# Performance work log

Hardware: AMD Instinct MI355X
Metric: run time of the kernel (lower is better)

## Reference

```python
import jax, jax.numpy as jnp
import numpy as np

N = 100000          # num_nodes
E = 1250000         # num_edges
H = 64              # node_hidden_size
T = 2               # num_rounds


def setup_inputs() -> dict:
    key = jax.random.key(0)
    ks = jax.random.split(key, 10)
    s = 0.1  # init scale for weights
    return {
        "x": jax.random.normal(ks[0], (N, H), dtype=jnp.float32),
        "edge_index": jax.random.randint(ks[1], (2, E), 0, N, dtype=jnp.int64),
        "edge_attr": jax.random.normal(ks[2], (E, 1), dtype=jnp.float32),
        # message layers: Linear(2H+1 -> H), one per round
        "msg_W": jax.random.normal(ks[3], (T, H, 2 * H + 1), dtype=jnp.float32) * s,
        "msg_b": jax.random.normal(ks[4], (T, H), dtype=jnp.float32) * s,
        # GRUCell params, gate order (r, z, n) as in torch
        "gru_Wih": jax.random.normal(ks[5], (T, 3 * H, H), dtype=jnp.float32) * s,
        "gru_bih": jax.random.normal(ks[6], (T, 3 * H), dtype=jnp.float32) * s,
        "gru_Whh": jax.random.normal(ks[7], (T, 3 * H, H), dtype=jnp.float32) * s,
        "gru_bhh": jax.random.normal(ks[8], (T, 3 * H), dtype=jnp.float32) * s,
    }


def _gru_cell(inp, h, Wih, bih, Whh, bhh):
    # torch.nn.GRUCell math, gate order r, z, n
    gi = inp @ Wih.T + bih   # [N, 3H]
    gh = h @ Whh.T + bhh     # [N, 3H]
    i_r, i_z, i_n = jnp.split(gi, 3, axis=1)
    h_r, h_z, h_n = jnp.split(gh, 3, axis=1)
    r = jax.nn.sigmoid(i_r + h_r)
    z = jax.nn.sigmoid(i_z + h_z)
    n = jnp.tanh(i_n + r * h_n)
    return (1.0 - z) * n + z * h


def reference(x, edge_index, edge_attr, msg_W, msg_b, gru_Wih, gru_bih, gru_Whh, gru_bhh):
    row, col = edge_index[0], edge_index[1]
    num_rounds = msg_W.shape[0]
    for t in range(num_rounds):
        src = x[row]    # [E, H]
        dest = x[col]   # [E, H]
        m_input = jnp.concatenate([dest, src, edge_attr], axis=1)  # [E, 2H+1]
        messages = m_input @ msg_W[t].T + msg_b[t]                 # [E, H]
        agg = jax.ops.segment_sum(messages, row, num_segments=x.shape[0])  # [N, H]
        x = _gru_cell(agg, x, gru_Wih[t], gru_bih[t], gru_Whh[t], gru_bhh[t])
    return x
```

## Files before the change

### kernel.cpp

```cpp
#include <hip/hip_runtime.h>
#include <hip/hip_bf16.h>
#include <hip/hip_fp16.h>

#define H 64
#define CAP 48

typedef __attribute__((ext_vector_type(8))) short short8;
typedef __attribute__((ext_vector_type(4))) float float4v;

__device__ __forceinline__ short f2bf_bits(float f) {
    union { __hip_bfloat16 b; short s; } u;
    u.b = __float2bfloat16(f);
    return u.s;
}
__device__ __forceinline__ float bf2f(unsigned short s) {
    union { unsigned int u; float f; } v;
    v.u = ((unsigned int)s) << 16;
    return v.f;
}
__device__ __forceinline__ void split8(const float* p, short8& hi, short8& lo) {
    float4v f0 = *(const float4v*)p;
    float4v f1 = *(const float4v*)(p + 4);
#pragma unroll
    for (int j = 0; j < 8; j++) {
        float f = (j < 4) ? f0[j] : f1[j - 4];
        short h = f2bf_bits(f);
        float fh = bf2f((unsigned short)h);
        hi[j] = h;
        lo[j] = f2bf_bits(f - fh);
    }
}
__device__ __forceinline__ void zero8(short8& hi, short8& lo) {
#pragma unroll
    for (int j = 0; j < 8; j++) { hi[j] = 0; lo[j] = 0; }
}

#define MFMA(a, b, c) __builtin_amdgcn_mfma_f32_16x16x32_bf16(a, b, c, 0, 0, 0)

__global__ __launch_bounds__(256) void count_prep(
    const int* __restrict__ row, int* __restrict__ deg, int* __restrict__ lpos,
    int E, int EB,
    const float* __restrict__ msg_W,
    const float* __restrict__ Wih, const float* __restrict__ Whh,
    short* __restrict__ msgfrag, short* __restrict__ grufrag, int T)
{
    if ((int)blockIdx.x < EB) {
        int e = blockIdx.x * 256 + threadIdx.x;
        if (e < E) lpos[e] = atomicAdd(&deg[row[e]], 1);
        return;
    }
    const int lane = threadIdx.x & 63;
    int unit = (blockIdx.x - EB) * 4 + (threadIdx.x >> 6);
    const int kq = (lane >> 4) * 8;
    if (unit < T * 16) {
        const int slot = unit & 15, t = unit >> 4;
        const int tile = slot >> 1, ks = slot & 1;
        const float* W = msg_W + (size_t)t * H * 129;
        const int wrow = (tile & 3) * 16 + (lane & 15);
        const int coff = (tile < 4) ? 0 : 64;
        short8 hi, lo;
        split8(W + (size_t)wrow * 129 + coff + ks * 32 + kq, hi, lo);
        short8* out = (short8*)(msgfrag + (size_t)t * 16384);
        out[slot * 64 + lane] = hi;
        out[16 * 64 + slot * 64 + lane] = lo;
    } else {
        unit -= T * 16;
        if (unit >= T * 48) return;
        const int slot = unit % 48, t = unit / 48;
        const int tile = slot >> 1, ks = slot & 1;
        const float* Wp = (tile < 12)
            ? (Wih + (size_t)t * 192 * H + ((size_t)(tile * 16 + (lane & 15))) * H)
            : (Whh + (size_t)t * 192 * H + ((size_t)((tile - 12) * 16 + (lane & 15))) * H);
        short8 hi, lo;
        split8(Wp + ks * 32 + kq, hi, lo);
        short8* out = (short8*)(grufrag + (size_t)t * 49152);
        out[slot * 64 + lane] = hi;
        out[48 * 64 + slot * 64 + lane] = lo;
    }
}

__global__ __launch_bounds__(256) void scatter_cast(
    const int* __restrict__ row, const int* __restrict__ col,
    const float* __restrict__ attr, const int* __restrict__ lpos,
    int2* __restrict__ edata, int E, int EB,
    const float* __restrict__ x_in, __half* __restrict__ xh, int NH8)
{
    if ((int)blockIdx.x < EB) {
        int e = blockIdx.x * 256 + threadIdx.x;
        if (e < E) {
            int p = lpos[e];
            if (p < CAP) {
                int2 v;
                v.x = col[e];
                v.y = __float_as_int(attr[e]);
                edata[(size_t)row[e] * CAP + p] = v;
            }
        }
    } else {
        int i = (blockIdx.x - EB) * 256 + threadIdx.x;
        if (i < NH8) {
            const float* p = x_in + (size_t)i * 8;
            float4v f0 = *(const float4v*)p;
            float4v f1 = *(const float4v*)(p + 4);
            short8 hv;
#pragma unroll
            for (int u = 0; u < 8; u++) {
                float f = (u < 4) ? f0[u] : f1[u - 4];
                hv[u] = __half_as_short(__float2half(f));
            }
            *(short8*)(xh + (size_t)i * 8) = hv;
        }
    }
}

#define SLD 68
__global__ __launch_bounds__(64) void agg_msg_gru(
    const int* __restrict__ deg, const int2* __restrict__ edata,
    const __half* __restrict__ xh_r,
    const float* xf,
    float* x, __half* __restrict__ xh_w,
    const short* __restrict__ mfrag, const short* __restrict__ gfrag,
    const float* __restrict__ Wt, const float* __restrict__ mb,
    const float* __restrict__ bih, const float* __restrict__ bhh,
    int N, int write_xh)
{
    __shared__ float scratch[16 * SLD];
    __shared__ float2 adeg[16];
    const int lane = threadIdx.x & 63;
    const int base = blockIdx.x * 16;
    if (base >= N) return;
    const int arow = lane & 15;
    const int kq = (lane >> 4) * 8;
    const int colb = lane & 15;
    const int rq4 = (lane >> 4) * 4;
    const int g = lane >> 3, cl = lane & 7;
    const short8* mhi = (const short8*)mfrag;
    const short8* mlo = mhi + 16 * 64;
    const short8* ghi = (const short8*)gfrag;
    const short8* glo = ghi + 48 * 64;

#pragma unroll
    for (int p = 0; p < 2; p++) {
        const int n = base + p * 8 + g;
        int cnt = 0;
        if (n < N) { cnt = deg[n]; if (cnt > CAP) cnt = CAP; }
        const int2* ebase = edata + (size_t)n * CAP;
        float acc[8] = {0.f,0.f,0.f,0.f,0.f,0.f,0.f,0.f};
        float aacc = 0.f;
        for (int j = 0; j < cnt; j += 8) {
            int2 e[8];
#pragma unroll
            for (int u = 0; u < 8; u++) {
                int idx = j + u; if (idx > cnt - 1) idx = cnt - 1;
                e[u] = ebase[idx];
            }
            short8 h[8];
#pragma unroll
            for (int u = 0; u < 8; u++) {
                int c = e[u].x;
                c = (c < 0) ? 0 : (c >= N ? N - 1 : c);
                h[u] = *(const short8*)(xh_r + (size_t)c * H + cl * 8);
            }
#pragma unroll
            for (int u = 0; u < 8; u++) {
                const bool val = (j + u < cnt);
                const float w = val ? 1.f : 0.f;
                aacc += val ? __int_as_float(e[u].y) : 0.f;
#pragma unroll
                for (int k = 0; k < 8; k++)
                    acc[k] = fmaf(w, __half2float(__ushort_as_half((unsigned short)h[u][k])), acc[k]);
            }
        }
        float* sr = scratch + (p * 8 + g) * SLD + cl * 8;
        *(float4v*)sr       = (float4v){acc[0], acc[1], acc[2], acc[3]};
        *(float4v*)(sr + 4) = (float4v){acc[4], acc[5], acc[6], acc[7]};
        if (cl == 0) adeg[p * 8 + g] = make_float2(aacc, (float)cnt);
    }
    asm volatile("s_waitcnt lgkmcnt(0)" ::: "memory");

    float2 da[4];
#pragma unroll
    for (int r = 0; r < 4; r++) da[r] = adeg[rq4 + r];

    const int m_a = base + arow;
    const bool mv = (m_a < N);
    short8 sfh[2], sfl[2], xfh[2], xfl[2];
#pragma unroll
    for (int ks = 0; ks < 2; ks++) {
        split8(scratch + arow * SLD + ks * 32 + kq, sfh[ks], sfl[ks]);
        if (mv) split8(xf + (size_t)m_a * H + ks * 32 + kq, xfh[ks], xfl[ks]);
        else    zero8(xfh[ks], xfl[ks]);
    }

#pragma unroll
    for (int ct = 0; ct < 4; ct++) {
        float4v accd = (float4v){0.f, 0.f, 0.f, 0.f};
        float4v accs = (float4v){0.f, 0.f, 0.f, 0.f};
#pragma unroll
        for (int ks = 0; ks < 2; ks++) {
            short8 bh = mhi[(ct * 2 + ks) * 64 + lane];
            short8 bl = mlo[(ct * 2 + ks) * 64 + lane];
            short8 ch = mhi[((4 + ct) * 2 + ks) * 64 + lane];
            short8 cl8 = mlo[((4 + ct) * 2 + ks) * 64 + lane];
            accd = MFMA(sfh[ks], bh, accd);
            accd = MFMA(sfl[ks], bh, accd);
            accd = MFMA(sfh[ks], bl, accd);
            accs = MFMA(xfh[ks], ch, accs);
            accs = MFMA(xfl[ks], ch, accs);
            accs = MFMA(xfh[ks], cl8, accs);
        }
        const int j = ct * 16 + colb;
        const float bj = mb[j];
        const float wa = Wt[(size_t)j * 129 + 128];
#pragma unroll
        for (int r = 0; r < 4; r++) {
            float v = accd[r] + da[r].y * (accs[r] + bj) + da[r].x * wa;
            scratch[(rq4 + r) * SLD + j] = v;
        }
    }
    asm volatile("s_waitcnt lgkmcnt(0)" ::: "memory");
    short8 agh[2], agl[2];
#pragma unroll
    for (int ks = 0; ks < 2; ks++)
        split8(scratch + arow * SLD + ks * 32 + kq, agh[ks], agl[ks]);

#pragma unroll
    for (int ct = 0; ct < 4; ct++) {
        float4v ai[3], ao[3];
#pragma unroll
        for (int g2 = 0; g2 < 3; g2++) {
            ai[g2] = (float4v){0.f, 0.f, 0.f, 0.f};
            ao[g2] = (float4v){0.f, 0.f, 0.f, 0.f};
        }
#pragma unroll
        for (int ks = 0; ks < 2; ks++) {
#pragma unroll
            for (int g2 = 0; g2 < 3; g2++) {
                short8 bh = ghi[((g2 * 4 + ct) * 2 + ks) * 64 + lane];
                short8 bl = glo[((g2 * 4 + ct) * 2 + ks) * 64 + lane];
                short8 hh = ghi[((12 + g2 * 4 + ct) * 2 + ks) * 64 + lane];
                short8 hl = glo[((12 + g2 * 4 + ct) * 2 + ks) * 64 + lane];
                ai[g2] = MFMA(agh[ks], bh, ai[g2]);
                ai[g2] = MFMA(agl[ks], bh, ai[g2]);
                ai[g2] = MFMA(agh[ks], bl, ai[g2]);
                ao[g2] = MFMA(xfh[ks], hh, ao[g2]);
                ao[g2] = MFMA(xfl[ks], hh, ao[g2]);
                ao[g2] = MFMA(xfh[ks], hl, ao[g2]);
            }
        }
        const int j = ct * 16 + colb;
        const float b_ir = bih[j], b_iz = bih[64 + j], b_in = bih[128 + j];
        const float b_hr = bhh[j], b_hz = bhh[64 + j], b_hn = bhh[128 + j];
#pragma unroll
        for (int r = 0; r < 4; r++) {
            const int m = base + rq4 + r;
            float ir = ai[0][r] + b_ir;
            float iz = ai[1][r] + b_iz;
            float in_ = ai[2][r] + b_in;
            float hr = ao[0][r] + b_hr;
            float hz = ao[1][r] + b_hz;
            float hn = ao[2][r] + b_hn;
            float rr = 1.f / (1.f + __expf(-(ir + hr)));
            float zz = 1.f / (1.f + __expf(-(iz + hz)));
            float e2 = __expf(2.f * (in_ + rr * hn));
            float nn = 1.f - 2.f / (e2 + 1.f);
            float hold = (m < N) ? xf[(size_t)m * H + j] : 0.f;
            scratch[(rq4 + r) * SLD + j] = (1.f - zz) * nn + zz * hold;
        }
    }
    asm volatile("s_waitcnt lgkmcnt(0)" ::: "memory");

    if (mv) {
        float4v o[4];
#pragma unroll
        for (int q4 = 0; q4 < 4; q4++)
            o[q4] = *(const float4v*)(scratch + arow * SLD + (lane >> 4) * 16 + q4 * 4);
        float4v* xp = (float4v*)(x + (size_t)m_a * H + (lane >> 4) * 16);
        xp[0] = o[0]; xp[1] = o[1]; xp[2] = o[2]; xp[3] = o[3];
        if (write_xh) {
            short8 hv0, hv1;
#pragma unroll
            for (int u = 0; u < 8; u++) {
                hv0[u] = __half_as_short(__float2half(o[u >> 2][u & 3]));
                hv1[u] = __half_as_short(__float2half(o[2 + (u >> 2)][u & 3]));
            }
            *(short8*)(xh_w + (size_t)m_a * H + (lane >> 4) * 16) = hv0;
            *(short8*)(xh_w + (size_t)m_a * H + (lane >> 4) * 16 + 8) = hv1;
        }
    }
}

extern "C" void kernel_launch(void* const* d_in, const int* in_sizes, int n_in,
                              void* d_out, int out_size, void* d_ws, size_t ws_size,
                              hipStream_t stream) {
    const float* x_in  = (const float*)d_in[0];
    const int*   ei    = (const int*)d_in[1];
    const float* attr  = (const float*)d_in[2];
    const float* msg_W = (const float*)d_in[3];
    const float* msg_b = (const float*)d_in[4];
    const float* Wih   = (const float*)d_in[5];
    const float* bih   = (const float*)d_in[6];
    const float* Whh   = (const float*)d_in[7];
    const float* bhh   = (const float*)d_in[8];

    const int N = in_sizes[0] / H;
    const int E = in_sizes[2];
    const int T = in_sizes[4] / H;
    const int* row = ei;
    const int* col = ei + E;

    float*  x       = (float*)d_out;
    __half* xh_a    = (__half*)d_ws;
    __half* xh_b    = xh_a + (size_t)N * H;
    int*    lpos    = (int*)(xh_b + (size_t)N * H);
    int*    deg     = lpos + E;
    int2*   edata   = (int2*)(deg + N);
    short*  msgfrag = (short*)(edata + (size_t)N * CAP);
    short*  grufrag = msgfrag + (size_t)T * 16384;

    const int eb  = (E + 255) / 256;
    const int nh8 = (N * H) / 8;
    const int cb  = (nh8 + 255) / 256;
    const int pb  = (T * 16 + T * 48 + 3) / 4;

    hipMemsetAsync(deg, 0, (size_t)N * sizeof(int), stream);

    count_prep<<<eb + pb, 256, 0, stream>>>(
        row, deg, lpos, E, eb, msg_W, Wih, Whh, msgfrag, grufrag, T);
    scatter_cast<<<eb + cb, 256, 0, stream>>>(
        row, col, attr, lpos, edata, E, eb, x_in, xh_a, nh8);

    const int mg_blocks = (N + 15) / 16;

    for (int t = 0; t < T; t++) {
        const __half* xh_r = (t & 1) ? xh_b : xh_a;
        __half*       xh_w = (t & 1) ? xh_a : xh_b;
        agg_msg_gru<<<mg_blocks, 64, 0, stream>>>(
            deg, edata, xh_r,
            (t == 0) ? x_in : x, x, xh_w,
            msgfrag + (size_t)t * 16384, grufrag + (size_t)t * 49152,
            msg_W + (size_t)t * H * (2 * H + 1), msg_b + (size_t)t * H,
            bih + (size_t)t * 3 * H, bhh + (size_t)t * 3 * H,
            N, (t + 1 < T) ? 1 : 0);
    }
}
```

Measured before the change: 318.5 us.

## Split edge counting and scatter into halves to overlap preprocessing phases

The atomic degree count and edge scatter now run in two halves. The first kernel counts the first half of the edges along with weight prep and the x cast. The second kernel counts the second half while scattering the first half, and a third kernel scatters the remainder. The aim is to overlap atomic counting with the scatter writes and cut idle tail time, at the cost of an extra kernel launch.

```diff
diff --git a/kernel.cpp b/kernel.cpp
--- a/kernel.cpp
+++ b/kernel.cpp
@@ -37,57 +37,79 @@
 
 #define MFMA(a, b, c) __builtin_amdgcn_mfma_f32_16x16x32_bf16(a, b, c, 0, 0, 0)
 
-__global__ __launch_bounds__(256) void count_prep(
+__global__ __launch_bounds__(256) void count_a(
     const int* __restrict__ row, int* __restrict__ deg, int* __restrict__ lpos,
-    int E, int EB,
+    int e1, int EB, int PB,
     const float* __restrict__ msg_W,
     const float* __restrict__ Wih, const float* __restrict__ Whh,
-    short* __restrict__ msgfrag, short* __restrict__ grufrag, int T)
-{
-    if ((int)blockIdx.x < EB) {
-        int e = blockIdx.x * 256 + threadIdx.x;
-        if (e < E) lpos[e] = atomicAdd(&deg[row[e]], 1);
-        return;
-    }
-    const int lane = threadIdx.x & 63;
-    int unit = (blockIdx.x - EB) * 4 + (threadIdx.x >> 6);
-    const int kq = (lane >> 4) * 8;
-    if (unit < T * 16) {
-        const int slot = unit & 15, t = unit >> 4;
-        const int tile = slot >> 1, ks = slot & 1;
-        const float* W = msg_W + (size_t)t * H * 129;
-        const int wrow = (tile & 3) * 16 + (lane & 15);
-        const int coff = (tile < 4) ? 0 : 64;
-        short8 hi, lo;
-        split8(W + (size_t)wrow * 129 + coff + ks * 32 + kq, hi, lo);
-        short8* out = (short8*)(msgfrag + (size_t)t * 16384);
-        out[slot * 64 + lane] = hi;
-        out[16 * 64 + slot * 64 + lane] = lo;
-    } else {
-        unit -= T * 16;
-        if (unit >= T * 48) return;
-        const int slot = unit % 48, t = unit / 48;
-        const int tile = slot >> 1, ks = slot & 1;
-        const float* Wp = (tile < 12)
-            ? (Wih + (size_t)t * 192 * H + ((size_t)(tile * 16 + (lane & 15))) * H)
-            : (Whh + (size_t)t * 192 * H + ((size_t)((tile - 12) * 16 + (lane & 15))) * H);
-        short8 hi, lo;
-        split8(Wp + ks * 32 + kq, hi, lo);
-        short8* out = (short8*)(grufrag + (size_t)t * 49152);
-        out[slot * 64 + lane] = hi;
-        out[48 * 64 + slot * 64 + lane] = lo;
-    }
-}
-
-__global__ __launch_bounds__(256) void scatter_cast(
-    const int* __restrict__ row, const int* __restrict__ col,
-    const float* __restrict__ attr, const int* __restrict__ lpos,
-    int2* __restrict__ edata, int E, int EB,
+    short* __restrict__ msgfrag, short* __restrict__ grufrag, int T,
     const float* __restrict__ x_in, __half* __restrict__ xh, int NH8)
 {
     if ((int)blockIdx.x < EB) {
         int e = blockIdx.x * 256 + threadIdx.x;
-        if (e < E) {
+        if (e < e1) lpos[e] = atomicAdd(&deg[row[e]], 1);
+        return;
+    }
+    int u = blockIdx.x - EB;
+    if (u < PB) {
+        const int lane = threadIdx.x & 63;
+        int unit = u * 4 + (threadIdx.x >> 6);
+        const int kq = (lane >> 4) * 8;
+        if (unit < T * 16) {
+            const int slot = unit & 15, t = unit >> 4;
+            const int tile = slot >> 1, ks = slot & 1;
+            const float* W = msg_W + (size_t)t * H * 129;
+            const int wrow = (tile & 3) * 16 + (lane & 15);
+            const int coff = (tile < 4) ? 0 : 64;
+            short8 hi, lo;
+            split8(W + (size_t)wrow * 129 + coff + ks * 32 + kq, hi, lo);
+            short8* out = (short8*)(msgfrag + (size_t)t * 16384);
+            out[slot * 64 + lane] = hi;
+            out[16 * 64 + slot * 64 + lane] = lo;
+        } else {
+            unit -= T * 16;
+            if (unit >= T * 48) return;
+            const int slot = unit % 48, t = unit / 48;
+            const int tile = slot >> 1, ks = slot & 1;
+            const float* Wp = (tile < 12)
+                ? (Wih + (size_t)t * 192 * H + ((size_t)(tile * 16 + (lane & 15))) * H)
+                : (Whh + (size_t)t * 192 * H + ((size_t)((tile - 12) * 16 + (lane & 15))) * H);
+            short8 hi, lo;
+            split8(Wp + ks * 32 + kq, hi, lo);
+            short8* out = (short8*)(grufrag + (size_t)t * 49152);
+            out[slot * 64 + lane] = hi;
+            out[48 * 64 + slot * 64 + lane] = lo;
+        }
+    } else {
+        int i = (u - PB) * 256 + threadIdx.x;
+        if (i < NH8) {
+            const float* p = x_in + (size_t)i * 8;
+            float4v f0 = *(const float4v*)p;
+            float4v f1 = *(const float4v*)(p + 4);
+            short8 hv;
+#pragma unroll
+            for (int v = 0; v < 8; v++) {
+                float f = (v < 4) ? f0[v] : f1[v - 4];
+                hv[v] = __half_as_short(__float2half(f));
+            }
+            *(short8*)(xh + (size_t)i * 8) = hv;
+        }
+    }
+}
+
+__global__ __launch_bounds__(256) void count_b(
+    const int* __restrict__ row, const int* __restrict__ col,
+    const float* __restrict__ attr,
+    int* __restrict__ deg, int* __restrict__ lpos,
+    int2* __restrict__ edata,
+    int c0, int E, int EBc, int s1)
+{
+    if ((int)blockIdx.x < EBc) {
+        int e = c0 + blockIdx.x * 256 + threadIdx.x;
+        if (e < E) lpos[e] = atomicAdd(&deg[row[e]], 1);
+    } else {
+        int e = (blockIdx.x - EBc) * 256 + threadIdx.x;
+        if (e < s1) {
             int p = lpos[e];
             if (p < CAP) {
                 int2 v;
@@ -96,19 +118,22 @@
                 edata[(size_t)row[e] * CAP + p] = v;
             }
         }
-    } else {
-        int i = (blockIdx.x - EB) * 256 + threadIdx.x;
-        if (i < NH8) {
-            const float* p = x_in + (size_t)i * 8;
-            float4v f0 = *(const float4v*)p;
-            float4v f1 = *(const float4v*)(p + 4);
-            short8 hv;
-#pragma unroll
-            for (int u = 0; u < 8; u++) {
-                float f = (u < 4) ? f0[u] : f1[u - 4];
-                hv[u] = __half_as_short(__float2half(f));
-            }
-            *(short8*)(xh + (size_t)i * 8) = hv;
+    }
+}
+
+__global__ __launch_bounds__(256) void scatter_b(
+    const int* __restrict__ row, const int* __restrict__ col,
+    const float* __restrict__ attr, const int* __restrict__ lpos,
+    int2* __restrict__ edata, int s0, int E)
+{
+    int e = s0 + blockIdx.x * 256 + threadIdx.x;
+    if (e < E) {
+        int p = lpos[e];
+        if (p < CAP) {
+            int2 v;
+            v.x = col[e];
+            v.y = __float_as_int(attr[e]);
+            edata[(size_t)row[e] * CAP + p] = v;
         }
     }
 }
@@ -318,17 +343,22 @@
     short*  msgfrag = (short*)(edata + (size_t)N * CAP);
     short*  grufrag = msgfrag + (size_t)T * 16384;
 
-    const int eb  = (E + 255) / 256;
     const int nh8 = (N * H) / 8;
     const int cb  = (nh8 + 255) / 256;
     const int pb  = (T * 16 + T * 48 + 3) / 4;
 
+    const int EB0 = (E / 2) / 256;
+    const int E0  = EB0 * 256;
+    const int EB1 = (E - E0 + 255) / 256;
+
     hipMemsetAsync(deg, 0, (size_t)N * sizeof(int), stream);
 
-    count_prep<<<eb + pb, 256, 0, stream>>>(
-        row, deg, lpos, E, eb, msg_W, Wih, Whh, msgfrag, grufrag, T);
-    scatter_cast<<<eb + cb, 256, 0, stream>>>(
-        row, col, attr, lpos, edata, E, eb, x_in, xh_a, nh8);
+    count_a<<<EB0 + pb + cb, 256, 0, stream>>>(
+        row, deg, lpos, E0, EB0, pb, msg_W, Wih, Whh, msgfrag, grufrag, T,
+        x_in, xh_a, nh8);
+    count_b<<<EB1 + EB0, 256, 0, stream>>>(
+        row, col, attr, deg, lpos, edata, E0, E, EB1, E0);
+    scatter_b<<<EB1, 256, 0, stream>>>(row, col, attr, lpos, edata, E0, E);
 
     const int mg_blocks = (N + 15) / 16;
 
```

After: 317.5 us. Within noise of the previous version (-0.3%).
